# Kernel tuning notes

Hardware: AMD Instinct MI355X
Metric: run time of the kernel (lower is better)

## Reference

```python
import jax, jax.numpy as jnp
import numpy as np

B, T, D = 32, 1024, 512
G, K = 8, 256          # num_groups, codes_per_group
GD = D // G            # group_dim = 64


def setup_inputs() -> dict:
    key = jax.random.key(0)
    k_x, k_cb = jax.random.split(key)
    x = jax.random.normal(k_x, (B, T, D), dtype=jnp.float32)
    # nn.Embedding weights init uniform_(-1/K, 1/K), one table per group -> [G, K, GD]
    codebooks = jax.random.uniform(k_cb, (G, K, GD), dtype=jnp.float32,
                                   minval=-1.0 / K, maxval=1.0 / K)
    return {"x": x, "codebooks": codebooks}


def reference(x, codebooks):
    Bx, Tx, Dx = x.shape
    xg = x.reshape(Bx, Tx, G, GD)                      # [B,T,G,gd]
    # squared euclidean distances to each code, per group: [B,T,G,K]
    x_sq = jnp.sum(xg ** 2, axis=-1, keepdims=True)    # [B,T,G,1]
    c_sq = jnp.sum(codebooks ** 2, axis=-1)            # [G,K]
    xc = jnp.einsum('btgd,gkd->btgk', xg, codebooks)   # [B,T,G,K]
    d = x_sq + c_sq[None, None] - 2.0 * xc
    idx = jnp.argmin(d, axis=-1)                       # [B,T,G] int
    # gather selected codes: codebooks[g, idx[b,t,g]] -> [B,T,G,gd]
    xq = jnp.take_along_axis(codebooks[None, None],    # [1,1,G,K,gd]
                             idx[..., None, None], axis=3).squeeze(3)
    sg = jax.lax.stop_gradient
    # per-group mse means (over B,T,gd), summed over groups (matches torch loop)
    losses = (jnp.sum(jnp.mean((sg(xq) - xg) ** 2, axis=(0, 1, 3)))
              + jnp.sum(jnp.mean((xq - sg(xg)) ** 2, axis=(0, 1, 3))))
    # straight-through estimator
    xq_st = xg + sg(xq - xg)
    x_q = xq_st.reshape(Bx, Tx, Dx)
    return x_q, losses, idx
```

## Files before the change

### kernel.cpp

```cpp
#include <hip/hip_runtime.h>

#define BT_TOTAL (32 * 1024)
#define DIM 512
#define NG 8
#define NK 256
#define GD 64
#define QB 128

#define XQ_ELEMS (BT_TOTAL * DIM)
#define LOSS_OFF XQ_ELEMS
#define IDX_OFF (XQ_ELEMS + 1)

__global__ void pq_prep(const float* __restrict__ cb,
                        float* __restrict__ csq,
                        float* __restrict__ loss_slot) {
    int i = blockIdx.x * 256 + threadIdx.x;
    if (i == 0) *loss_slot = 0.0f;
    if (i < NG * NK) {
        const float* row = cb + (size_t)i * GD;
        float a0 = 0.f, a1 = 0.f, a2 = 0.f, a3 = 0.f;
#pragma unroll
        for (int d = 0; d < GD; d += 4) {
            a0 = fmaf(row[d + 0], row[d + 0], a0);
            a1 = fmaf(row[d + 1], row[d + 1], a1);
            a2 = fmaf(row[d + 2], row[d + 2], a2);
            a3 = fmaf(row[d + 3], row[d + 3], a3);
        }
        csq[i] = (a0 + a1) + (a2 + a3);
    }
}

__global__ __launch_bounds__(256, 4) void pq_main(const float* __restrict__ x,
                                                  const float* __restrict__ cb,
                                                  const float* __restrict__ csq,
                                                  float* __restrict__ out) {
    const int g = blockIdx.y;
    const int t = threadIdx.x;
    const int kh = __builtin_amdgcn_readfirstlane(t >> 7);
    const int ql = t & (QB - 1);
    const int q0 = blockIdx.x * QB;
    const int bt = q0 + ql;

    __shared__ float m_d[QB];
    __shared__ int   m_i[QB];
    __shared__ float wsum[4];

    const float* xrow = x + (size_t)bt * DIM + g * GD;
    float4 xr[16];
#pragma unroll
    for (int i = 0; i < 16; ++i) xr[i] = ((const float4*)xrow)[i];

    float a0 = 0.f, a1 = 0.f, a2 = 0.f, a3 = 0.f;
#pragma unroll
    for (int i = 0; i < 16; ++i) {
        a0 = fmaf(xr[i].x, xr[i].x, a0);
        a1 = fmaf(xr[i].y, xr[i].y, a1);
        a2 = fmaf(xr[i].z, xr[i].z, a2);
        a3 = fmaf(xr[i].w, xr[i].w, a3);
    }
    const float x_sq = (a0 + a1) + (a2 + a3);

    const float* cbg = cb + (size_t)g * NK * GD;
    const float* csqg = csq + g * NK;

    const int kbase = kh << 7;
    float best = 3.402823466e38f;
    int bi = kbase;
#pragma unroll 2
    for (int kk = 0; kk < 128; ++kk) {
        const int k = kbase + kk;
        const float4* c4 = (const float4*)(cbg + k * GD);
        float d0 = 0.f, d1 = 0.f, d2 = 0.f, d3 = 0.f;
#pragma unroll
        for (int i = 0; i < 16; ++i) {
            float4 c = c4[i];
            d0 = fmaf(xr[i].x, c.x, d0);
            d1 = fmaf(xr[i].y, c.y, d1);
            d2 = fmaf(xr[i].z, c.z, d2);
            d3 = fmaf(xr[i].w, c.w, d3);
        }
        float dot = (d0 + d1) + (d2 + d3);
        float dist = (x_sq + csqg[k]) - 2.0f * dot;
        if (dist < best) { best = dist; bi = k; }
    }

    if (kh == 1) { m_d[ql] = best; m_i[ql] = bi; }
    __syncthreads();
    if (kh == 0) {
        float dh = m_d[ql];
        int ih = m_i[ql];
        if (dh < best) { best = dh; bi = ih; }
        m_i[ql] = bi;
        out[IDX_OFF + (size_t)bt * NG + g] = (float)bi;
    }
    __syncthreads();

    const int r_off = t >> 4;
    const int c4i = t & 15;
    float s0 = 0.f, s1 = 0.f, s2 = 0.f, s3 = 0.f;
#pragma unroll
    for (int p = 0; p < 8; ++p) {
        const int r = p * 16 + r_off;
        const int code = m_i[r];
        const size_t base = (size_t)(q0 + r) * DIM + g * GD + c4i * 4;
        float4 x4 = *(const float4*)(x + base);
        float4 q4 = *(const float4*)(cbg + code * GD + c4i * 4);
        float dx = q4.x - x4.x;
        float dy = q4.y - x4.y;
        float dz = q4.z - x4.z;
        float dw = q4.w - x4.w;
        float4 o;
        o.x = x4.x + dx;
        o.y = x4.y + dy;
        o.z = x4.z + dz;
        o.w = x4.w + dw;
        *(float4*)(out + base) = o;
        s0 = fmaf(dx, dx, s0);
        s1 = fmaf(dy, dy, s1);
        s2 = fmaf(dz, dz, s2);
        s3 = fmaf(dw, dw, s3);
    }
    float part = (s0 + s1) + (s2 + s3);

#pragma unroll
    for (int off = 32; off > 0; off >>= 1) part += __shfl_down(part, off);

    const int lane = t & 63;
    const int wid = t >> 6;
    if (lane == 0) wsum[wid] = part;
    __syncthreads();
    if (t == 0) {
        float bs = (wsum[0] + wsum[1]) + (wsum[2] + wsum[3]);
        atomicAdd(out + LOSS_OFF, bs * (2.0f / 2097152.0f));
    }
}

extern "C" void kernel_launch(void* const* d_in, const int* in_sizes, int n_in,
                              void* d_out, int out_size, void* d_ws, size_t ws_size,
                              hipStream_t stream) {
    const float* x = (const float*)d_in[0];
    const float* cb = (const float*)d_in[1];
    float* out = (float*)d_out;
    float* csq = (float*)d_ws;

    pq_prep<<<dim3(8), dim3(256), 0, stream>>>(cb, csq, out + LOSS_OFF);

    dim3 grid(BT_TOTAL / QB, NG);
    pq_main<<<grid, dim3(256), 0, stream>>>(x, cb, csq, out);
}
```

Measured before the change: 147.5 us.

## Tile distance computation through LDS with 4x8 register blocking per thread

```diff
diff --git a/kernel.cpp b/kernel.cpp
--- a/kernel.cpp
+++ b/kernel.cpp
@@ -5,7 +5,13 @@
 #define NG 8
 #define NK 256
 #define GD 64
+
 #define QB 128
+#define CCH 64
+#define NCH 4
+
+#define XT_STRIDE 65
+#define CT_STRIDE 68
 
 #define XQ_ELEMS (BT_TOTAL * DIM)
 #define LOSS_OFF XQ_ELEMS
@@ -30,68 +36,169 @@
     }
 }
 
-__global__ __launch_bounds__(256, 4) void pq_main(const float* __restrict__ x,
+__global__ __launch_bounds__(256, 3) void pq_main(const float* __restrict__ x,
                                                   const float* __restrict__ cb,
                                                   const float* __restrict__ csq,
                                                   float* __restrict__ out) {
     const int g = blockIdx.y;
     const int t = threadIdx.x;
-    const int kh = __builtin_amdgcn_readfirstlane(t >> 7);
-    const int ql = t & (QB - 1);
     const int q0 = blockIdx.x * QB;
-    const int bt = q0 + ql;
-
-    __shared__ float m_d[QB];
+
+    __shared__ __align__(16) float ct[GD * CT_STRIDE];
+    __shared__ __align__(16) float xt[QB * XT_STRIDE];
+    __shared__ float xsq[QB];
     __shared__ int   m_i[QB];
     __shared__ float wsum[4];
 
-    const float* xrow = x + (size_t)bt * DIM + g * GD;
-    float4 xr[16];
-#pragma unroll
-    for (int i = 0; i < 16; ++i) xr[i] = ((const float4*)xrow)[i];
-
-    float a0 = 0.f, a1 = 0.f, a2 = 0.f, a3 = 0.f;
-#pragma unroll
-    for (int i = 0; i < 16; ++i) {
-        a0 = fmaf(xr[i].x, xr[i].x, a0);
-        a1 = fmaf(xr[i].y, xr[i].y, a1);
-        a2 = fmaf(xr[i].z, xr[i].z, a2);
-        a3 = fmaf(xr[i].w, xr[i].w, a3);
-    }
-    const float x_sq = (a0 + a1) + (a2 + a3);
-
     const float* cbg = cb + (size_t)g * NK * GD;
     const float* csqg = csq + g * NK;
-
-    const int kbase = kh << 7;
-    float best = 3.402823466e38f;
-    int bi = kbase;
-#pragma unroll 2
-    for (int kk = 0; kk < 128; ++kk) {
-        const int k = kbase + kk;
-        const float4* c4 = (const float4*)(cbg + k * GD);
-        float d0 = 0.f, d1 = 0.f, d2 = 0.f, d3 = 0.f;
+    const float* xg = x + (size_t)q0 * DIM + g * GD;
+
+#pragma unroll
+    for (int j = 0; j < 8; ++j) {
+        int flat = t + j * 256;
+        int q = flat >> 4;
+        int dv = flat & 15;
+        float4 v = *(const float4*)(xg + (size_t)q * DIM + dv * 4);
+        float* w = &xt[q * XT_STRIDE + dv * 4];
+        w[0] = v.x; w[1] = v.y; w[2] = v.z; w[3] = v.w;
+    }
+#pragma unroll
+    for (int j = 0; j < 4; ++j) {
+        int flat = t + j * 256;
+        int c = flat >> 4;
+        int dv = flat & 15;
+        float4 v = *(const float4*)(cbg + (size_t)c * GD + dv * 4);
+        ct[(dv * 4 + 0) * CT_STRIDE + c] = v.x;
+        ct[(dv * 4 + 1) * CT_STRIDE + c] = v.y;
+        ct[(dv * 4 + 2) * CT_STRIDE + c] = v.z;
+        ct[(dv * 4 + 3) * CT_STRIDE + c] = v.w;
+    }
+    if (t < QB) {
+        const float4* xr4 = (const float4*)(xg + (size_t)t * DIM);
+        float a0 = 0.f, a1 = 0.f, a2 = 0.f, a3 = 0.f;
 #pragma unroll
         for (int i = 0; i < 16; ++i) {
-            float4 c = c4[i];
-            d0 = fmaf(xr[i].x, c.x, d0);
-            d1 = fmaf(xr[i].y, c.y, d1);
-            d2 = fmaf(xr[i].z, c.z, d2);
-            d3 = fmaf(xr[i].w, c.w, d3);
-        }
-        float dot = (d0 + d1) + (d2 + d3);
-        float dist = (x_sq + csqg[k]) - 2.0f * dot;
-        if (dist < best) { best = dist; bi = k; }
-    }
-
-    if (kh == 1) { m_d[ql] = best; m_i[ql] = bi; }
-    __syncthreads();
-    if (kh == 0) {
-        float dh = m_d[ql];
-        int ih = m_i[ql];
-        if (dh < best) { best = dh; bi = ih; }
-        m_i[ql] = bi;
-        out[IDX_OFF + (size_t)bt * NG + g] = (float)bi;
+            float4 v = xr4[i];
+            a0 = fmaf(v.x, v.x, a0);
+            a1 = fmaf(v.y, v.y, a1);
+            a2 = fmaf(v.z, v.z, a2);
+            a3 = fmaf(v.w, v.w, a3);
+        }
+        xsq[t] = (a0 + a1) + (a2 + a3);
+    }
+    __syncthreads();
+
+    const int tx = t & 7;
+    const int ty = t >> 3;
+    const int qb = ty * 4;
+
+    float best[4], bidx_f;
+    int bidx[4];
+#pragma unroll
+    for (int j = 0; j < 4; ++j) { best[j] = 3.402823466e38f; bidx[j] = 0; }
+    (void)bidx_f;
+
+    for (int ch = 0; ch < NCH; ++ch) {
+        const int c0 = ch * CCH;
+        float acc[4][8];
+#pragma unroll
+        for (int j = 0; j < 4; ++j)
+#pragma unroll
+            for (int i = 0; i < 8; ++i) acc[j][i] = 0.f;
+
+        const float* xrow = &xt[qb * XT_STRIDE];
+        const float* cbase = &ct[tx * 8];
+#pragma unroll 8
+        for (int d = 0; d < GD; ++d) {
+            float xv0 = xrow[0 * XT_STRIDE + d];
+            float xv1 = xrow[1 * XT_STRIDE + d];
+            float xv2 = xrow[2 * XT_STRIDE + d];
+            float xv3 = xrow[3 * XT_STRIDE + d];
+            float4 cA = *(const float4*)(cbase + d * CT_STRIDE);
+            float4 cB = *(const float4*)(cbase + d * CT_STRIDE + 4);
+            acc[0][0] = fmaf(xv0, cA.x, acc[0][0]);
+            acc[0][1] = fmaf(xv0, cA.y, acc[0][1]);
+            acc[0][2] = fmaf(xv0, cA.z, acc[0][2]);
+            acc[0][3] = fmaf(xv0, cA.w, acc[0][3]);
+            acc[0][4] = fmaf(xv0, cB.x, acc[0][4]);
+            acc[0][5] = fmaf(xv0, cB.y, acc[0][5]);
+            acc[0][6] = fmaf(xv0, cB.z, acc[0][6]);
+            acc[0][7] = fmaf(xv0, cB.w, acc[0][7]);
+            acc[1][0] = fmaf(xv1, cA.x, acc[1][0]);
+            acc[1][1] = fmaf(xv1, cA.y, acc[1][1]);
+            acc[1][2] = fmaf(xv1, cA.z, acc[1][2]);
+            acc[1][3] = fmaf(xv1, cA.w, acc[1][3]);
+            acc[1][4] = fmaf(xv1, cB.x, acc[1][4]);
+            acc[1][5] = fmaf(xv1, cB.y, acc[1][5]);
+            acc[1][6] = fmaf(xv1, cB.z, acc[1][6]);
+            acc[1][7] = fmaf(xv1, cB.w, acc[1][7]);
+            acc[2][0] = fmaf(xv2, cA.x, acc[2][0]);
+            acc[2][1] = fmaf(xv2, cA.y, acc[2][1]);
+            acc[2][2] = fmaf(xv2, cA.z, acc[2][2]);
+            acc[2][3] = fmaf(xv2, cA.w, acc[2][3]);
+            acc[2][4] = fmaf(xv2, cB.x, acc[2][4]);
+            acc[2][5] = fmaf(xv2, cB.y, acc[2][5]);
+            acc[2][6] = fmaf(xv2, cB.z, acc[2][6]);
+            acc[2][7] = fmaf(xv2, cB.w, acc[2][7]);
+            acc[3][0] = fmaf(xv3, cA.x, acc[3][0]);
+            acc[3][1] = fmaf(xv3, cA.y, acc[3][1]);
+            acc[3][2] = fmaf(xv3, cA.z, acc[3][2]);
+            acc[3][3] = fmaf(xv3, cA.w, acc[3][3]);
+            acc[3][4] = fmaf(xv3, cB.x, acc[3][4]);
+            acc[3][5] = fmaf(xv3, cB.y, acc[3][5]);
+            acc[3][6] = fmaf(xv3, cB.z, acc[3][6]);
+            acc[3][7] = fmaf(xv3, cB.w, acc[3][7]);
+        }
+
+#pragma unroll
+        for (int j = 0; j < 4; ++j) {
+            float xs = xsq[qb + j];
+#pragma unroll
+            for (int i = 0; i < 8; ++i) {
+                int k = c0 + tx * 8 + i;
+                float dist = (xs + csqg[k]) - 2.0f * acc[j][i];
+                if (dist < best[j]) { best[j] = dist; bidx[j] = k; }
+            }
+        }
+
+        __syncthreads();
+        if (ch < NCH - 1) {
+            const int c0n = (ch + 1) * CCH;
+#pragma unroll
+            for (int j = 0; j < 4; ++j) {
+                int flat = t + j * 256;
+                int c = flat >> 4;
+                int dv = flat & 15;
+                float4 v = *(const float4*)(cbg + (size_t)(c0n + c) * GD + dv * 4);
+                ct[(dv * 4 + 0) * CT_STRIDE + c] = v.x;
+                ct[(dv * 4 + 1) * CT_STRIDE + c] = v.y;
+                ct[(dv * 4 + 2) * CT_STRIDE + c] = v.z;
+                ct[(dv * 4 + 3) * CT_STRIDE + c] = v.w;
+            }
+            __syncthreads();
+        }
+    }
+
+    float* red_d = ct;
+    int*   red_i = (int*)(ct + 8 * QB);
+#pragma unroll
+    for (int j = 0; j < 4; ++j) {
+        red_d[tx * QB + qb + j] = best[j];
+        red_i[tx * QB + qb + j] = bidx[j];
+    }
+    __syncthreads();
+    if (t < QB) {
+        float b = red_d[t];
+        int bi = red_i[t];
+#pragma unroll
+        for (int s = 1; s < 8; ++s) {
+            float v = red_d[s * QB + t];
+            int vi = red_i[s * QB + t];
+            if (v < b || (v == b && vi < bi)) { b = v; bi = vi; }
+        }
+        m_i[t] = bi;
+        out[IDX_OFF + (size_t)(q0 + t) * NG + g] = (float)bi;
     }
     __syncthreads();
 
@@ -102,19 +209,19 @@
     for (int p = 0; p < 8; ++p) {
         const int r = p * 16 + r_off;
         const int code = m_i[r];
-        const size_t base = (size_t)(q0 + r) * DIM + g * GD + c4i * 4;
-        float4 x4 = *(const float4*)(x + base);
-        float4 q4 = *(const float4*)(cbg + code * GD + c4i * 4);
-        float dx = q4.x - x4.x;
-        float dy = q4.y - x4.y;
-        float dz = q4.z - x4.z;
-        float dw = q4.w - x4.w;
+        const float* xls = &xt[r * XT_STRIDE + c4i * 4];
+        float x0 = xls[0], x1 = xls[1], x2 = xls[2], x3 = xls[3];
+        float4 q4 = *(const float4*)(cbg + (size_t)code * GD + c4i * 4);
+        float dx = q4.x - x0;
+        float dy = q4.y - x1;
+        float dz = q4.z - x2;
+        float dw = q4.w - x3;
         float4 o;
-        o.x = x4.x + dx;
-        o.y = x4.y + dy;
-        o.z = x4.z + dz;
-        o.w = x4.w + dw;
-        *(float4*)(out + base) = o;
+        o.x = x0 + dx;
+        o.y = x1 + dy;
+        o.z = x2 + dz;
+        o.w = x3 + dw;
+        *(float4*)(out + (size_t)(q0 + r) * DIM + g * GD + c4i * 4) = o;
         s0 = fmaf(dx, dx, s0);
         s1 = fmaf(dy, dy, s1);
         s2 = fmaf(dz, dz, s2);
```

After: 144.7 us. No clear change (-1.9%).

## Load codebook rows via scalar loads and give each thread all 256 codes

Applied to the files above, without the earlier changes.

```diff
diff --git a/kernel.cpp b/kernel.cpp
--- a/kernel.cpp
+++ b/kernel.cpp
@@ -5,11 +5,13 @@
 #define NG 8
 #define NK 256
 #define GD 64
-#define QB 128
+#define QB 256
 
 #define XQ_ELEMS (BT_TOTAL * DIM)
 #define LOSS_OFF XQ_ELEMS
 #define IDX_OFF (XQ_ELEMS + 1)
+
+typedef float f32x16 __attribute__((ext_vector_type(16)));
 
 __global__ void pq_prep(const float* __restrict__ cb,
                         float* __restrict__ csq,
@@ -36,14 +38,14 @@
                                                   float* __restrict__ out) {
     const int g = blockIdx.y;
     const int t = threadIdx.x;
-    const int kh = __builtin_amdgcn_readfirstlane(t >> 7);
-    const int ql = t & (QB - 1);
     const int q0 = blockIdx.x * QB;
-    const int bt = q0 + ql;
+    const int bt = q0 + t;
 
-    __shared__ float m_d[QB];
     __shared__ int   m_i[QB];
     __shared__ float wsum[4];
+
+    const float* cbg = cb + (size_t)g * NK * GD;
+    const float* csqg = csq + g * NK;
 
     const float* xrow = x + (size_t)bt * DIM + g * GD;
     float4 xr[16];
@@ -60,51 +62,56 @@
     }
     const float x_sq = (a0 + a1) + (a2 + a3);
 
-    const float* cbg = cb + (size_t)g * NK * GD;
-    const float* csqg = csq + g * NK;
+    float best = 3.402823466e38f;
+    int bi = 0;
 
-    const int kbase = kh << 7;
-    float best = 3.402823466e38f;
-    int bi = kbase;
-#pragma unroll 2
-    for (int kk = 0; kk < 128; ++kk) {
-        const int k = kbase + kk;
-        const float4* c4 = (const float4*)(cbg + k * GD);
+#pragma unroll 1
+    for (int k = 0; k < NK; ++k) {
+        f32x16 c0, c1, c2, c3;
+        float cs;
+        const float* ck = cbg + (size_t)k * GD;
+        const float* pk = csqg + k;
+        asm volatile(
+            "s_load_dwordx16 %0, %5, 0x0\n\t"
+            "s_load_dwordx16 %1, %5, 0x40\n\t"
+            "s_load_dwordx16 %2, %5, 0x80\n\t"
+            "s_load_dwordx16 %3, %5, 0xc0\n\t"
+            "s_load_dword    %4, %6, 0x0"
+            : "=s"(c0), "=s"(c1), "=s"(c2), "=s"(c3), "=s"(cs)
+            : "s"(ck), "s"(pk));
+        asm volatile("s_waitcnt lgkmcnt(0)"
+                     : "+s"(c0), "+s"(c1), "+s"(c2), "+s"(c3), "+s"(cs));
+
         float d0 = 0.f, d1 = 0.f, d2 = 0.f, d3 = 0.f;
-#pragma unroll
-        for (int i = 0; i < 16; ++i) {
-            float4 c = c4[i];
-            d0 = fmaf(xr[i].x, c.x, d0);
-            d1 = fmaf(xr[i].y, c.y, d1);
-            d2 = fmaf(xr[i].z, c.z, d2);
-            d3 = fmaf(xr[i].w, c.w, d3);
-        }
+#define Q4(cv, i4, b)                              \
+        d0 = fmaf(cv[(i4) * 4 + 0], xr[b].x, d0);  \
+        d1 = fmaf(cv[(i4) * 4 + 1], xr[b].y, d1);  \
+        d2 = fmaf(cv[(i4) * 4 + 2], xr[b].z, d2);  \
+        d3 = fmaf(cv[(i4) * 4 + 3], xr[b].w, d3);
+        Q4(c0, 0, 0)  Q4(c0, 1, 1)  Q4(c0, 2, 2)  Q4(c0, 3, 3)
+        Q4(c1, 0, 4)  Q4(c1, 1, 5)  Q4(c1, 2, 6)  Q4(c1, 3, 7)
+        Q4(c2, 0, 8)  Q4(c2, 1, 9)  Q4(c2, 2, 10) Q4(c2, 3, 11)
+        Q4(c3, 0, 12) Q4(c3, 1, 13) Q4(c3, 2, 14) Q4(c3, 3, 15)
+#undef Q4
         float dot = (d0 + d1) + (d2 + d3);
-        float dist = (x_sq + csqg[k]) - 2.0f * dot;
+        float dist = (x_sq + cs) - 2.0f * dot;
         if (dist < best) { best = dist; bi = k; }
     }
 
-    if (kh == 1) { m_d[ql] = best; m_i[ql] = bi; }
-    __syncthreads();
-    if (kh == 0) {
-        float dh = m_d[ql];
-        int ih = m_i[ql];
-        if (dh < best) { best = dh; bi = ih; }
-        m_i[ql] = bi;
-        out[IDX_OFF + (size_t)bt * NG + g] = (float)bi;
-    }
+    m_i[t] = bi;
+    out[IDX_OFF + (size_t)bt * NG + g] = (float)bi;
     __syncthreads();
 
     const int r_off = t >> 4;
     const int c4i = t & 15;
     float s0 = 0.f, s1 = 0.f, s2 = 0.f, s3 = 0.f;
 #pragma unroll
-    for (int p = 0; p < 8; ++p) {
+    for (int p = 0; p < 16; ++p) {
         const int r = p * 16 + r_off;
         const int code = m_i[r];
         const size_t base = (size_t)(q0 + r) * DIM + g * GD + c4i * 4;
         float4 x4 = *(const float4*)(x + base);
-        float4 q4 = *(const float4*)(cbg + code * GD + c4i * 4);
+        float4 q4 = *(const float4*)(cbg + (size_t)code * GD + c4i * 4);
         float dx = q4.x - x4.x;
         float dy = q4.y - x4.y;
         float dz = q4.z - x4.z;
```

After: 129.8 us. 1.14x faster.
